# Kernel optimization log

Measured on AMD Instinct MI355X. Metric: run time of the kernel, lower is better.

Reference implementation:

```python
import jax, jax.numpy as jnp
import numpy as np

N_NODES = 20000


def _segment_softmax(alpha, dst, num_nodes):
    # numerically-stable softmax over edges grouped by destination node
    m = jax.ops.segment_max(alpha, dst, num_segments=num_nodes)
    m = jnp.where(jnp.isfinite(m), m, 0.0)
    a = jnp.exp(alpha - m[dst])
    denom = jax.ops.segment_sum(a, dst, num_segments=num_nodes)
    return a / denom[dst]


def mgcn_conv(x, src, dst, edge_type, basis, att, weight, root, bias, num_nodes):
    # x: [N, in], basis: [B, in, out], att: [R, B], weight: [R, out=in]
    x_i = x[dst]                                   # [E, in] target feats
    x_j = x[src]                                   # [E, in] source feats
    # per-edge attention logit: sum_d x_i[d] * w_r[d] * x_j[d]
    alpha = jnp.sum(x_i * weight[edge_type] * x_j, axis=1)   # [E]
    alpha = _segment_softmax(alpha, dst, num_nodes)          # [E]
    # basis-decomposed per-edge transform: x_j @ (att_r . basis)
    t = jnp.einsum('ei,bio->ebo', x_j, basis)                # [E, B, out]
    msg = jnp.einsum('ebo,eb->eo', t, att[edge_type])        # [E, out]
    msg = msg * alpha[:, None]
    out = jax.ops.segment_sum(msg, dst, num_segments=num_nodes)  # [N, out]
    return out + x @ root + bias


def setup_inputs() -> dict:
    key = jax.random.key(0)
    ks = jax.random.split(key, 16)
    E, D, R, B, N = 32768, 128, 474, 64, N_NODES
    s = 0.05
    return {
        'entity': jnp.arange(N, dtype=jnp.int64) if jax.config.jax_enable_x64 else jnp.arange(N, dtype=jnp.int32),
        'edge_index': jax.random.randint(ks[0], (2, E), 0, N, dtype=jnp.int32),
        'edge_type': jax.random.randint(ks[1], (E,), 0, R, dtype=jnp.int32),
        'emb_table': jax.random.normal(ks[2], (N, D), dtype=jnp.float32),
        'basis1': jax.random.normal(ks[3], (B, D, D), dtype=jnp.float32) * s,
        'att1': jax.random.normal(ks[4], (R, B), dtype=jnp.float32) * s,
        'weight1': jax.random.normal(ks[5], (R, D), dtype=jnp.float32) * s,
        'root1': jax.random.normal(ks[6], (D, D), dtype=jnp.float32) * s,
        'bias1': jnp.zeros((D,), dtype=jnp.float32),
        'basis2': jax.random.normal(ks[7], (B, D, D), dtype=jnp.float32) * s,
        'att2': jax.random.normal(ks[8], (R, B), dtype=jnp.float32) * s,
        'weight2': jax.random.normal(ks[9], (R, D), dtype=jnp.float32) * s,
        'root2': jax.random.normal(ks[10], (D, D), dtype=jnp.float32) * s,
        'bias2': jnp.zeros((D,), dtype=jnp.float32),
    }


def reference(entity, edge_index, edge_type, emb_table,
              basis1, att1, weight1, root1, bias1,
              basis2, att2, weight2, root2, bias2):
    src, dst = edge_index[0], edge_index[1]   # PyG: (source j, target i)
    x = emb_table[entity]                     # embedding lookup
    h = jax.nn.relu(mgcn_conv(x, src, dst, edge_type, basis1, att1,
                              weight1, root1, bias1, N_NODES))
    # dropout is identity at inference
    out = mgcn_conv(h, src, dst, edge_type, basis2, att2,
                    weight2, root2, bias2, N_NODES)
    return out
```

## Files before the change

kernel.cpp:

```cpp
#include <hip/hip_runtime.h>
#include <hip/hip_bf16.h>

#define N_NODES 20000
#define N_EDGES 32768
#define DIM 128
#define N_REL 474
#define N_BASIS 64
#define TILE_E 64
#define WSTRIDE 264
#define LELIST 512

#define WMIX_BLKS 1024
#define ROOTT_BLKS 2
#define GATHER_BASE (WMIX_BLKS + ROOTT_BLKS)
#define PREP_GRID 1664

#define MSG_REL_BLKS (2 * N_REL)
#define RG_BLKS ((N_NODES + 63) / 64)
#define MSG_GRID (MSG_REL_BLKS + RG_BLKS)
#define MERGE_GRID 1024

typedef __bf16 bf16x8 __attribute__((ext_vector_type(8)));
typedef float f32x4 __attribute__((ext_vector_type(4)));

__device__ __forceinline__ unsigned short f2b(float f) {
    unsigned u = __float_as_uint(f);
    unsigned r = (u + 0x7FFFu + ((u >> 16) & 1u)) >> 16;
    return (unsigned short)r;
}
__device__ __forceinline__ float b2f(unsigned short s) {
    return __uint_as_float(((unsigned)s) << 16);
}
__device__ __forceinline__ __bf16 u2b(unsigned short u) {
    union { unsigned short u; __bf16 b; } c; c.u = u; return c.b;
}
__device__ __forceinline__ float dot2bf(unsigned a, unsigned b, float wx, float wy) {
    return b2f((unsigned short)(a & 0xFFFFu)) * wx * b2f((unsigned short)(b & 0xFFFFu))
         + b2f((unsigned short)(a >> 16)) * wy * b2f((unsigned short)(b >> 16));
}

__global__ __launch_bounds__(256) void prep_kernel(const float4* __restrict__ emb,
                                                   const int* __restrict__ entity,
                                                   ushort4* __restrict__ xb4,
                                                   float4* __restrict__ zreg, int zcount4,
                                                   const float* __restrict__ att1,
                                                   const float* __restrict__ basis1,
                                                   unsigned short* __restrict__ W1,
                                                   const float* __restrict__ att2,
                                                   const float* __restrict__ basis2,
                                                   unsigned short* __restrict__ W2,
                                                   const float* __restrict__ root1,
                                                   unsigned short* __restrict__ rootT1,
                                                   const float* __restrict__ root2,
                                                   unsigned short* __restrict__ rootT2) {
    __shared__ __align__(16) unsigned short bt[64 * WSTRIDE];
    int t = threadIdx.x;
    if (blockIdx.x < WMIX_BLKS) {
        int wi = blockIdx.x;
        int layer = wi >> 9;
        int cb = (wi >> 3) & 63;
        int rg = wi & 7;
        const float* att   = layer ? att2 : att1;
        const float* basis = layer ? basis2 : basis1;
        unsigned short* W  = layer ? W2 : W1;
        int io0 = cb * 256;
        int r0 = rg * 64;
#pragma unroll
        for (int p = 0; p < 16; p++) {
            int c = t + 256 * p;
            int k = c >> 6, of = c & 63;
            float4 v = *(const float4*)(basis + (size_t)k * (DIM * DIM) + io0 + of * 4);
            ushort4 s;
            s.x = f2b(v.x); s.y = f2b(v.y); s.z = f2b(v.z); s.w = f2b(v.w);
            int ofx = of ^ (((k >> 3) & 7) << 2);
            *(ushort4*)&bt[k * WSTRIDE + ofx * 4] = s;
        }
        __syncthreads();

        int w = t >> 6, l = t & 63, n = l & 15, q = l >> 4;
        bf16x8 bfr[2][4];
#pragma unroll
        for (int kb = 0; kb < 2; kb++) {
            int kbase = kb * 32 + q * 8;
            int sx = ((kb * 4 + q) & 7) << 4;
#pragma unroll
            for (int c = 0; c < 4; c++) {
                int ob = (w * 64 + c * 16 + n) ^ sx;
#pragma unroll
                for (int j = 0; j < 8; j++) bfr[kb][c][j] = u2b(bt[(kbase + j) * WSTRIDE + ob]);
            }
        }
        __syncthreads();

        f32x4 acc[4][4] = {};
#pragma unroll
        for (int kb = 0; kb < 2; kb++) {
            int kbase = kb * 32 + q * 8;
            bf16x8 a[4];
#pragma unroll
            for (int rt = 0; rt < 4; rt++) {
                int rm = min(r0 + rt * 16 + n, N_REL - 1);
                const float4* ap = (const float4*)(att + (size_t)rm * N_BASIS + kbase);
                float4 u0 = ap[0], u1 = ap[1];
                a[rt][0] = (__bf16)u0.x; a[rt][1] = (__bf16)u0.y;
                a[rt][2] = (__bf16)u0.z; a[rt][3] = (__bf16)u0.w;
                a[rt][4] = (__bf16)u1.x; a[rt][5] = (__bf16)u1.y;
                a[rt][6] = (__bf16)u1.z; a[rt][7] = (__bf16)u1.w;
            }
#pragma unroll
            for (int c = 0; c < 4; c++) {
#pragma unroll
                for (int rt = 0; rt < 4; rt++)
                    acc[rt][c] = __builtin_amdgcn_mfma_f32_16x16x32_bf16(a[rt], bfr[kb][c], acc[rt][c], 0, 0, 0);
            }
        }
#pragma unroll
        for (int rt = 0; rt < 4; rt++) {
#pragma unroll
            for (int c = 0; c < 4; c++) {
#pragma unroll
                for (int g = 0; g < 4; g++)
                    bt[(rt * 16 + q * 4 + g) * WSTRIDE + w * 64 + c * 16 + n] = f2b(acc[rt][c][g]);
            }
        }
        __syncthreads();
        int srow = t >> 2, sseg = t & 3;
        int rr = r0 + srow;
        if (rr < N_REL) {
            const int4* sp = (const int4*)&bt[srow * WSTRIDE];
            unsigned short* wp = W + (size_t)rr * (DIM * DIM) + io0;
#pragma unroll
            for (int ii = 0; ii < 8; ii++) {
                int i = (ii + sseg * 2) & 7;
                int4 v = sp[sseg * 8 + i];
                *(int4*)(wp + sseg * 64 + i * 8) = v;
            }
        }
    } else if (blockIdx.x < GATHER_BASE) {
        int wi2 = blockIdx.x - WMIX_BLKS;
        const float* rm = wi2 ? root2 : root1;
        unsigned short* rt_ = wi2 ? rootT2 : rootT1;
        unsigned short* sb16 = bt;
#pragma unroll
        for (int p = 0; p < 16; p++) {
            int idx = t + 256 * p;
            int k = idx >> 5, o4 = idx & 31;
            float4 v = ((const float4*)rm)[idx];
            ushort4 s;
            s.x = f2b(v.x); s.y = f2b(v.y); s.z = f2b(v.z); s.w = f2b(v.w);
            *(ushort4*)&sb16[k * 132 + o4 * 4] = s;
        }
        __syncthreads();
        int o = t >> 1, kh = (t & 1) * 64;
#pragma unroll
        for (int i = 0; i < 16; i++) {
            int k0 = kh + i * 4;
            ushort4 s;
            s.x = sb16[(k0 + 0) * 132 + o];
            s.y = sb16[(k0 + 1) * 132 + o];
            s.z = sb16[(k0 + 2) * 132 + o];
            s.w = sb16[(k0 + 3) * 132 + o];
            *(ushort4*)&rt_[o * DIM + k0] = s;
        }
    } else {
        int pb = blockIdx.x - GATHER_BASE;
        int gtid = pb * 256 + t;
        int gsz = (PREP_GRID - GATHER_BASE) * 256;
        int total4 = N_NODES * DIM / 4;
        for (int i = gtid; i < total4; i += gsz) {
            int n = i >> 5, rem = i & 31;
            float4 v = emb[(size_t)entity[n] * 32 + rem];
            ushort4 s;
            s.x = f2b(v.x); s.y = f2b(v.y); s.z = f2b(v.z); s.w = f2b(v.w);
            xb4[i] = s;
        }
        float4 z = make_float4(0.f, 0.f, 0.f, 0.f);
        for (int i = gtid; i < zcount4; i += gsz) zreg[i] = z;
    }
}

__global__ __launch_bounds__(256) void msg_kernel(const unsigned short* __restrict__ xb,
                                                  const unsigned short* __restrict__ W,
                                                  const float* __restrict__ wlog,
                                                  const int* __restrict__ src,
                                                  const int* __restrict__ dst,
                                                  const int* __restrict__ etype,
                                                  float* __restrict__ den,
                                                  float* __restrict__ accm,
                                                  const unsigned short* __restrict__ rootT,
                                                  float* __restrict__ racc) {
    __shared__ __align__(16) unsigned short wt[128 * 136];
    __shared__ __align__(16) float wf[DIM];
    __shared__ float scf[TILE_E];
    __shared__ int sdd[TILE_E];
    __shared__ int ssrc[TILE_E];
    __shared__ int elist[LELIST];
    __shared__ int lcnt;

    int t = threadIdx.x;
    if ((int)blockIdx.x < MSG_REL_BLKS) {
        int r = blockIdx.x >> 1, half = blockIdx.x & 1;
        const unsigned short* Wr = W + (size_t)r * (DIM * DIM);
        if (t == 0) lcnt = 0;
#pragma unroll
        for (int p = 0; p < 8; p++) {
            int c = t + 256 * p;
            int k = c >> 4, oct = c & 15;
            int4 v = *(const int4*)(Wr + k * DIM + oct * 8);
            int oct2 = oct ^ (((k >> 3) & 7) << 1);
            *(int4*)&wt[k * 136 + oct2 * 8] = v;
        }
        if (t < 32) ((float4*)wf)[t] = ((const float4*)(wlog + (size_t)r * DIM))[t];
        __syncthreads();

        int lane = t & 63;
        for (int it = half * 16; it < half * 16 + 16; it++) {
            int idx = it * 256 + t;
            int4 ev = ((const int4*)etype)[idx];
#pragma unroll
            for (int j = 0; j < 4; j++) {
                int etj = (j == 0) ? ev.x : (j == 1) ? ev.y : (j == 2) ? ev.z : ev.w;
                bool m = (etj == r);
                unsigned long long bal = __ballot(m);
                int tot = __popcll(bal);
                if (tot) {
                    int base = 0;
                    if (lane == 0) base = atomicAdd(&lcnt, tot);
                    base = __shfl(base, 0, 64);
                    if (m) {
                        int pre = __popcll(bal & ((1ull << lane) - 1ull));
                        int p_ = base + pre;
                        if (p_ < LELIST) elist[p_] = idx * 4 + j;
                    }
                }
            }
        }
        __syncthreads();
        int cnt = min(lcnt, LELIST);
        if (cnt == 0) return;

        int w = t >> 6, l = t & 63, n = l & 15, q = l >> 4;
        int el4 = t >> 2, l4 = t & 3;

        for (int t0 = 0; t0 < cnt; t0 += TILE_E) {
            int nE = min(TILE_E, cnt - t0);
            if (t < TILE_E) {
                if (t < nE) {
                    int e = elist[t0 + t];
                    ssrc[t] = src[e];
                    sdd[t]  = dst[e];
                } else { ssrc[t] = 0; sdd[t] = 0; }
            }
            __syncthreads();

            {
                int s_ = ssrc[el4], d_ = sdd[el4];
                const int4* xj = (const int4*)(xb + (size_t)s_ * DIM) + l4 * 4;
                const int4* xi = (const int4*)(xb + (size_t)d_ * DIM) + l4 * 4;
                const float4* wv = (const float4*)&wf[l4 * 32];
                float v = 0.f;
#pragma unroll
                for (int u = 0; u < 4; u++) {
                    int4 a = xj[u]; int4 bb = xi[u];
                    float4 w0 = wv[u * 2], w1 = wv[u * 2 + 1];
                    v += dot2bf((unsigned)a.x, (unsigned)bb.x, w0.x, w0.y)
                       + dot2bf((unsigned)a.y, (unsigned)bb.y, w0.z, w0.w)
                       + dot2bf((unsigned)a.z, (unsigned)bb.z, w1.x, w1.y)
                       + dot2bf((unsigned)a.w, (unsigned)bb.w, w1.z, w1.w);
                }
                v += __shfl_xor(v, 1, 64);
                v += __shfl_xor(v, 2, 64);
                if (l4 == 0) {
                    if (el4 < nE) {
                        float a = expf(v);
                        scf[el4] = a;
                        atomicAdd(&den[d_], a);
                    } else scf[el4] = 0.f;
                }
            }
            __syncthreads();

            f32x4 acc[2][4] = {};
#pragma unroll
            for (int kb = 0; kb < 4; kb++) {
                bf16x8 a[4];
#pragma unroll
                for (int rt = 0; rt < 4; rt++)
                    a[rt] = *(const bf16x8*)(xb + (size_t)ssrc[rt * 16 + n] * DIM + kb * 32 + q * 8);
                int kbase = kb * 32 + q * 8;
                int sx = ((kb * 4 + q) & 7) << 4;
#pragma unroll
                for (int c = 0; c < 2; c++) {
                    int ob = ((w * 2 + c) * 16 + n) ^ sx;
                    bf16x8 bb;
#pragma unroll
                    for (int j = 0; j < 8; j++) bb[j] = u2b(wt[(kbase + j) * 136 + ob]);
#pragma unroll
                    for (int rt = 0; rt < 4; rt++)
                        acc[c][rt] = __builtin_amdgcn_mfma_f32_16x16x32_bf16(a[rt], bb, acc[c][rt], 0, 0, 0);
                }
            }
#pragma unroll
            for (int c = 0; c < 2; c++) {
                int col = (w * 2 + c) * 16 + n;
#pragma unroll
                for (int rt = 0; rt < 4; rt++) {
#pragma unroll
                    for (int rg = 0; rg < 4; rg++) {
                        int e = rt * 16 + q * 4 + rg;
                        if (e < nE)
                            atomicAdd(&accm[(size_t)sdd[e] * DIM + col], scf[e] * acc[c][rt][rg]);
                    }
                }
            }
            __syncthreads();
        }
    } else {
        int n0 = ((int)blockIdx.x - MSG_REL_BLKS) * 64;
        unsigned short* xrf = wt;
#pragma unroll
        for (int p = 0; p < 4; p++) {
            int c = t + 256 * p;
            int g = c >> 6;
            int rt = g >> 2, kb = g & 3;
            int q2 = (c >> 4) & 3, m = c & 15;
            int row = n0 + rt * 16 + m;
            int oct = kb * 4 + q2;
            int4 v = make_int4(0, 0, 0, 0);
            if (row < N_NODES) v = *(const int4*)(xb + (size_t)row * DIM + oct * 8);
            *(int4*)&xrf[c * 8] = v;
        }
        __syncthreads();

        int w_ = t >> 6, l = t & 63, n = l & 15, q = l >> 4;
        f32x4 acc[2][4] = {};
#pragma unroll
        for (int kb = 0; kb < 4; kb++) {
            bf16x8 a[4];
#pragma unroll
            for (int rt = 0; rt < 4; rt++) a[rt] = *(const bf16x8*)&xrf[((rt * 4 + kb) * 64 + l) * 8];
            int kbase = kb * 32 + q * 8;
#pragma unroll
            for (int c = 0; c < 2; c++) {
                int col = (w_ * 2 + c) * 16 + n;
                bf16x8 bb = *(const bf16x8*)(rootT + (size_t)col * DIM + kbase);
#pragma unroll
                for (int rt = 0; rt < 4; rt++)
                    acc[c][rt] = __builtin_amdgcn_mfma_f32_16x16x32_bf16(a[rt], bb, acc[c][rt], 0, 0, 0);
            }
        }
#pragma unroll
        for (int c = 0; c < 2; c++) {
            int col = (w_ * 2 + c) * 16 + n;
#pragma unroll
            for (int rt = 0; rt < 4; rt++) {
#pragma unroll
                for (int rg = 0; rg < 4; rg++) {
                    int row = n0 + rt * 16 + q * 4 + rg;
                    if (row < N_NODES)
                        racc[(size_t)row * DIM + col] = acc[c][rt][rg];
                }
            }
        }
    }
}

__global__ __launch_bounds__(256) void merge_kernel(const float4* __restrict__ racc,
                                                    const float4* __restrict__ accm,
                                                    const float* __restrict__ den,
                                                    const float* __restrict__ bias,
                                                    float4* __restrict__ outf,
                                                    ushort4* __restrict__ outb) {
    int gtid = blockIdx.x * 256 + threadIdx.x;
    const int tot4 = N_NODES * (DIM / 4);
    for (int i = gtid; i < tot4; i += (int)gridDim.x * 256) {
        int row = i >> 5;
        int c0 = (i & 31) * 4;
        float4 rv = racc[i];
        float4 mv = accm[i];
        float4 bo = *(const float4*)&bias[c0];
        float dv = den[row];
        float inv = dv > 0.f ? 1.0f / dv : 0.f;
        float4 v;
        v.x = rv.x + bo.x + mv.x * inv;
        v.y = rv.y + bo.y + mv.y * inv;
        v.z = rv.z + bo.z + mv.z * inv;
        v.w = rv.w + bo.w + mv.w * inv;
        if (outb) {
            ushort4 s;
            s.x = f2b(fmaxf(v.x, 0.f)); s.y = f2b(fmaxf(v.y, 0.f));
            s.z = f2b(fmaxf(v.z, 0.f)); s.w = f2b(fmaxf(v.w, 0.f));
            outb[i] = s;
        } else {
            outf[i] = v;
        }
    }
}

extern "C" void kernel_launch(void* const* d_in, const int* in_sizes, int n_in,
                              void* d_out, int out_size, void* d_ws, size_t ws_size,
                              hipStream_t stream) {
    const int N = N_NODES, E = N_EDGES, R = N_REL;

    const int* entity = (const int*)d_in[0];
    const int* eidx   = (const int*)d_in[1];
    const int* src    = eidx;
    const int* dst    = eidx + E;
    const int* etype  = (const int*)d_in[2];
    const float* emb  = (const float*)d_in[3];
    const float* basis1 = (const float*)d_in[4];
    const float* att1   = (const float*)d_in[5];
    const float* w1     = (const float*)d_in[6];
    const float* root1  = (const float*)d_in[7];
    const float* bias1  = (const float*)d_in[8];
    const float* basis2 = (const float*)d_in[9];
    const float* att2   = (const float*)d_in[10];
    const float* w2     = (const float*)d_in[11];
    const float* root2  = (const float*)d_in[12];
    const float* bias2  = (const float*)d_in[13];
    float* out = (float*)d_out;

    size_t off = 0;
    auto alloc = [&](size_t bytes) -> void* {
        void* p = (char*)d_ws + off;
        off += (bytes + 255) & ~(size_t)255;
        return p;
    };
    unsigned short* W1 = (unsigned short*)alloc((size_t)R * DIM * DIM * 2);
    unsigned short* W2 = (unsigned short*)alloc((size_t)R * DIM * DIM * 2);
    unsigned short* xb = (unsigned short*)alloc((size_t)N * DIM * 2);
    unsigned short* hb = (unsigned short*)alloc((size_t)N * DIM * 2);
    float* racc1  = (float*)alloc((size_t)N * DIM * 4);
    float* racc2  = (float*)alloc((size_t)N * DIM * 4);
    float* zreg   = (float*)alloc(((size_t)2 * N + (size_t)2 * N * DIM) * 4);
    float* den1   = zreg;
    float* den2   = zreg + N;
    float* accm1  = zreg + 2 * N;
    float* accm2  = zreg + 2 * N + (size_t)N * DIM;
    unsigned short* rootT1 = (unsigned short*)alloc((size_t)DIM * DIM * 2);
    unsigned short* rootT2 = (unsigned short*)alloc((size_t)DIM * DIM * 2);

    int zcount4 = (2 * N + 2 * N * DIM) / 4;

    prep_kernel<<<PREP_GRID, 256, 0, stream>>>(
        (const float4*)emb, entity, (ushort4*)xb, (float4*)zreg, zcount4,
        att1, basis1, W1, att2, basis2, W2, root1, rootT1, root2, rootT2);

    msg_kernel<<<MSG_GRID, 256, 0, stream>>>(xb, W1, w1, src, dst, etype,
                                             den1, accm1, rootT1, racc1);
    merge_kernel<<<MERGE_GRID, 256, 0, stream>>>((const float4*)racc1, (const float4*)accm1,
                                                 den1, bias1, nullptr, (ushort4*)hb);

    msg_kernel<<<MSG_GRID, 256, 0, stream>>>(hb, W2, w2, src, dst, etype,
                                             den2, accm2, rootT2, racc2);
    merge_kernel<<<MERGE_GRID, 256, 0, stream>>>((const float4*)racc2, (const float4*)accm2,
                                                 den2, bias2, (float4*)out, nullptr);
}
```

Before: 212.7 us.

## Bucket edges by relation with histogram, scan and scatter into fixed chunks

Replaces the per-block scan of all edge types (each of 948 blocks reading 16K etypes and ballot-compacting) with a histogram built in prep, a single-block prefix scan producing per-relation offsets and fixed-size chunk descriptors, and a scatter kernel that writes edge ids grouped by relation. msg_kernel blocks then read their relation's edge list directly and are assigned per chunk of at most 128 edges, which removes the redundant etype scans and the 512-edge cap. The cost is two extra small kernel launches plus global atomics in the scatter, and edge order within a relation now depends on atomic timing.

```diff
diff --git a/kernel.cpp b/kernel.cpp
--- a/kernel.cpp
+++ b/kernel.cpp
@@ -7,17 +7,19 @@
 #define N_REL 474
 #define N_BASIS 64
 #define TILE_E 64
+#define CHCAP 128
+#define MAXCH (N_EDGES / CHCAP + N_REL)
 #define WSTRIDE 264
-#define LELIST 512
+#define HIST_BLKS 16
+#define EDGES_PER_HIST (N_EDGES / HIST_BLKS)
 
 #define WMIX_BLKS 1024
 #define ROOTT_BLKS 2
 #define GATHER_BASE (WMIX_BLKS + ROOTT_BLKS)
 #define PREP_GRID 1664
 
-#define MSG_REL_BLKS (2 * N_REL)
 #define RG_BLKS ((N_NODES + 63) / 64)
-#define MSG_GRID (MSG_REL_BLKS + RG_BLKS)
+#define MSG_GRID (MAXCH + RG_BLKS)
 #define MERGE_GRID 1024
 
 typedef __bf16 bf16x8 __attribute__((ext_vector_type(8)));
@@ -41,8 +43,10 @@
 
 __global__ __launch_bounds__(256) void prep_kernel(const float4* __restrict__ emb,
                                                    const int* __restrict__ entity,
+                                                   const int* __restrict__ etype,
                                                    ushort4* __restrict__ xb4,
                                                    float4* __restrict__ zreg, int zcount4,
+                                                   int* __restrict__ partial,
                                                    const float* __restrict__ att1,
                                                    const float* __restrict__ basis1,
                                                    unsigned short* __restrict__ W1,
@@ -176,6 +180,58 @@
         }
         float4 z = make_float4(0.f, 0.f, 0.f, 0.f);
         for (int i = gtid; i < zcount4; i += gsz) zreg[i] = z;
+        if (pb < HIST_BLKS) {
+            int* ih = (int*)bt;
+            for (int i = t; i < N_REL; i += 256) ih[i] = 0;
+            __syncthreads();
+            int e0 = pb * EDGES_PER_HIST;
+            for (int e = e0 + t; e < e0 + EDGES_PER_HIST; e += 256)
+                atomicAdd(&ih[etype[e]], 1);
+            __syncthreads();
+            for (int i = t; i < N_REL; i += 256) partial[pb * N_REL + i] = ih[i];
+        }
+    }
+}
+
+__global__ void scanr_kernel(const int* __restrict__ partial, int* __restrict__ offs,
+                             int* __restrict__ cursor, int* __restrict__ chunk_r,
+                             int* __restrict__ chunk_o, int* __restrict__ nchunks) {
+    __shared__ int s[512];
+    __shared__ int lnc;
+    int t = threadIdx.x;
+    int v = 0;
+    if (t < N_REL) {
+#pragma unroll
+        for (int k = 0; k < HIST_BLKS; k++) v += partial[k * N_REL + t];
+    }
+    s[t] = v;
+    if (t == 0) lnc = 0;
+    __syncthreads();
+    for (int d = 1; d < 512; d <<= 1) {
+        int add = (t >= d) ? s[t - d] : 0;
+        __syncthreads();
+        s[t] += add;
+        __syncthreads();
+    }
+    int excl = s[t] - v;
+    if (t < N_REL) { offs[t] = excl; cursor[t] = excl; }
+    if (t == 0) offs[N_REL] = N_EDGES;
+    if (t < N_REL && v > 0) {
+        int nc = (v + CHCAP - 1) / CHCAP;
+        int cb = atomicAdd(&lnc, nc);
+        for (int c = 0; c < nc; c++) { chunk_r[cb + c] = t; chunk_o[cb + c] = excl + c * CHCAP; }
+    }
+    __syncthreads();
+    if (t == 0) *nchunks = lnc;
+}
+
+__global__ __launch_bounds__(256) void scatter_kernel(const int* __restrict__ etype,
+                                                      int* __restrict__ cursor,
+                                                      int* __restrict__ eids) {
+    for (int e = blockIdx.x * 256 + threadIdx.x; e < N_EDGES; e += (int)gridDim.x * 256) {
+        int r = etype[e];
+        int p = atomicAdd(&cursor[r], 1);
+        eids[p] = e;
     }
 }
 
@@ -184,7 +240,11 @@
                                                   const float* __restrict__ wlog,
                                                   const int* __restrict__ src,
                                                   const int* __restrict__ dst,
-                                                  const int* __restrict__ etype,
+                                                  const int* __restrict__ eids,
+                                                  const int* __restrict__ offs,
+                                                  const int* __restrict__ chunk_r,
+                                                  const int* __restrict__ chunk_o,
+                                                  const int* __restrict__ nchunks,
                                                   float* __restrict__ den,
                                                   float* __restrict__ accm,
                                                   const unsigned short* __restrict__ rootT,
@@ -194,14 +254,14 @@
     __shared__ float scf[TILE_E];
     __shared__ int sdd[TILE_E];
     __shared__ int ssrc[TILE_E];
-    __shared__ int elist[LELIST];
-    __shared__ int lcnt;
 
     int t = threadIdx.x;
-    if ((int)blockIdx.x < MSG_REL_BLKS) {
-        int r = blockIdx.x >> 1, half = blockIdx.x & 1;
+    if ((int)blockIdx.x < MAXCH) {
+        if ((int)blockIdx.x >= *nchunks) return;
+        int r = chunk_r[blockIdx.x];
+        int base = chunk_o[blockIdx.x];
+        int cnt = min(base + CHCAP, offs[r + 1]) - base;
         const unsigned short* Wr = W + (size_t)r * (DIM * DIM);
-        if (t == 0) lcnt = 0;
 #pragma unroll
         for (int p = 0; p < 8; p++) {
             int c = t + 256 * p;
@@ -213,32 +273,6 @@
         if (t < 32) ((float4*)wf)[t] = ((const float4*)(wlog + (size_t)r * DIM))[t];
         __syncthreads();
 
-        int lane = t & 63;
-        for (int it = half * 16; it < half * 16 + 16; it++) {
-            int idx = it * 256 + t;
-            int4 ev = ((const int4*)etype)[idx];
-#pragma unroll
-            for (int j = 0; j < 4; j++) {
-                int etj = (j == 0) ? ev.x : (j == 1) ? ev.y : (j == 2) ? ev.z : ev.w;
-                bool m = (etj == r);
-                unsigned long long bal = __ballot(m);
-                int tot = __popcll(bal);
-                if (tot) {
-                    int base = 0;
-                    if (lane == 0) base = atomicAdd(&lcnt, tot);
-                    base = __shfl(base, 0, 64);
-                    if (m) {
-                        int pre = __popcll(bal & ((1ull << lane) - 1ull));
-                        int p_ = base + pre;
-                        if (p_ < LELIST) elist[p_] = idx * 4 + j;
-                    }
-                }
-            }
-        }
-        __syncthreads();
-        int cnt = min(lcnt, LELIST);
-        if (cnt == 0) return;
-
         int w = t >> 6, l = t & 63, n = l & 15, q = l >> 4;
         int el4 = t >> 2, l4 = t & 3;
 
@@ -246,7 +280,7 @@
             int nE = min(TILE_E, cnt - t0);
             if (t < TILE_E) {
                 if (t < nE) {
-                    int e = elist[t0 + t];
+                    int e = eids[base + t0 + t];
                     ssrc[t] = src[e];
                     sdd[t]  = dst[e];
                 } else { ssrc[t] = 0; sdd[t] = 0; }
@@ -316,7 +350,7 @@
             __syncthreads();
         }
     } else {
-        int n0 = ((int)blockIdx.x - MSG_REL_BLKS) * 64;
+        int n0 = ((int)blockIdx.x - MAXCH) * 64;
         unsigned short* xrf = wt;
 #pragma unroll
         for (int p = 0; p < 4; p++) {
@@ -439,19 +473,31 @@
     float* accm2  = zreg + 2 * N + (size_t)N * DIM;
     unsigned short* rootT1 = (unsigned short*)alloc((size_t)DIM * DIM * 2);
     unsigned short* rootT2 = (unsigned short*)alloc((size_t)DIM * DIM * 2);
+    int* partial  = (int*)alloc((size_t)HIST_BLKS * R * 4);
+    int* offs     = (int*)alloc((size_t)(R + 1) * 4);
+    int* cursor   = (int*)alloc((size_t)R * 4);
+    int* eids     = (int*)alloc((size_t)E * 4);
+    int* chunk_r  = (int*)alloc((size_t)MAXCH * 4);
+    int* chunk_o  = (int*)alloc((size_t)MAXCH * 4);
+    int* nchunks  = (int*)alloc(256);
 
     int zcount4 = (2 * N + 2 * N * DIM) / 4;
 
     prep_kernel<<<PREP_GRID, 256, 0, stream>>>(
-        (const float4*)emb, entity, (ushort4*)xb, (float4*)zreg, zcount4,
+        (const float4*)emb, entity, etype, (ushort4*)xb, (float4*)zreg, zcount4, partial,
         att1, basis1, W1, att2, basis2, W2, root1, rootT1, root2, rootT2);
 
-    msg_kernel<<<MSG_GRID, 256, 0, stream>>>(xb, W1, w1, src, dst, etype,
+    scanr_kernel<<<1, 512, 0, stream>>>(partial, offs, cursor, chunk_r, chunk_o, nchunks);
+    scatter_kernel<<<64, 256, 0, stream>>>(etype, cursor, eids);
+
+    msg_kernel<<<MSG_GRID, 256, 0, stream>>>(xb, W1, w1, src, dst, eids, offs,
+                                             chunk_r, chunk_o, nchunks,
                                              den1, accm1, rootT1, racc1);
     merge_kernel<<<MERGE_GRID, 256, 0, stream>>>((const float4*)racc1, (const float4*)accm1,
                                                  den1, bias1, nullptr, (ushort4*)hb);
 
-    msg_kernel<<<MSG_GRID, 256, 0, stream>>>(hb, W2, w2, src, dst, etype,
+    msg_kernel<<<MSG_GRID, 256, 0, stream>>>(hb, W2, w2, src, dst, eids, offs,
+                                             chunk_r, chunk_o, nchunks,
                                              den2, accm2, rootT2, racc2);
     merge_kernel<<<MERGE_GRID, 256, 0, stream>>>((const float4*)racc2, (const float4*)accm2,
                                                  den2, bias2, (float4*)out, nullptr);
```

Result: no change. 212.0 us (-0.3%).
